# Kernel tuning notes

Measured on AMD Instinct MI355X. Metric: run time of the kernel, lower is better.

## Reference

```python
import jax, jax.numpy as jnp
import numpy as np

NUM_USERS = 100000
NUM_ITEMS = 100000
N = NUM_USERS + NUM_ITEMS
D = 64
E = 3200000


def setup_inputs() -> dict:
    key = jax.random.key(0)
    ks = jax.random.split(key, 8)
    edge_index = jax.random.randint(ks[0], (2, E), 0, N, dtype=jnp.int64)
    edge_weight = jax.random.uniform(ks[1], (E,), dtype=jnp.float32)
    user_emb = jax.random.normal(ks[2], (NUM_USERS, D), dtype=jnp.float32) * 0.1
    item_emb = jax.random.normal(ks[3], (NUM_ITEMS, D), dtype=jnp.float32) * 0.1
    s = 1.0 / np.sqrt(D)
    W1 = jax.random.uniform(ks[4], (D, D), dtype=jnp.float32, minval=-s, maxval=s)
    b1 = jax.random.uniform(ks[5], (D,), dtype=jnp.float32, minval=-s, maxval=s)
    W2 = jax.random.uniform(ks[6], (D, D), dtype=jnp.float32, minval=-s, maxval=s)
    b2 = jax.random.uniform(ks[7], (D,), dtype=jnp.float32, minval=-s, maxval=s)
    return {"edge_index": edge_index, "edge_weight": edge_weight,
            "user_emb": user_emb, "item_emb": item_emb,
            "W1": W1, "b1": b1, "W2": W2, "b2": b2}


def _gcn_layer(x, src, dst, edge_weight, W, b):
    # message: edge_weight * x[src]; aggregate: scatter-add at dst
    msg = edge_weight[:, None] * x[src]              # [E, D] gather + mul
    agg = jax.ops.segment_sum(msg, dst, num_segments=N)  # [N, D] scatter-add
    updated = (agg + x) * 0.5                        # residual average
    return updated @ W + b                           # linear


def reference(edge_index, edge_weight, user_emb, item_emb, W1, b1, W2, b2):
    src = edge_index[0]
    dst = edge_index[1]
    x = jnp.concatenate([user_emb, item_emb], axis=0)  # [N, D]
    x = _gcn_layer(x, src, dst, edge_weight, W1, b1)
    x = _gcn_layer(x, src, dst, edge_weight, W2, b2)
    return x
```

## Files before the change

kernel.cpp:

```cpp
#include <hip/hip_runtime.h>
#include <hip/hip_fp16.h>

#define NUM_USERS 100000
#define NN        200000
#define DD        64
#define EE        3200000
#define SCAN_CHUNK 2048
#define NB_SCAN   98

#define KB_   391
#define GSEG  512
#define EPS   (EE / GSEG)
#define MSEG  (KB_ * GSEG)

typedef _Float16 half8 __attribute__((ext_vector_type(8)));
typedef _Float16 half4 __attribute__((ext_vector_type(4)));
typedef float    f32x4 __attribute__((ext_vector_type(4)));

__global__ __launch_bounds__(256) void scan_partials_kernel(
    const int* __restrict__ counts, int* __restrict__ bsum, int len)
{
    __shared__ int s[256];
    const int t = threadIdx.x;
    int sum = 0;
    for (int i = t; i < SCAN_CHUNK; i += 256) {
        const int idx = blockIdx.x * SCAN_CHUNK + i;
        sum += (idx < len) ? counts[idx] : 0;
    }
    s[t] = sum; __syncthreads();
    for (int off = 128; off > 0; off >>= 1) {
        if (t < off) s[t] += s[t + off];
        __syncthreads();
    }
    if (t == 0) bsum[blockIdx.x] = s[0];
}

__global__ __launch_bounds__(128) void scan_top_kernel(int* __restrict__ bsum, int nb)
{
    __shared__ int s[128];
    const int t = threadIdx.x;
    const int v = (t < nb) ? bsum[t] : 0;
    s[t] = v; __syncthreads();
    for (int off = 1; off < 128; off <<= 1) {
        int add = (t >= off) ? s[t - off] : 0;
        __syncthreads();
        s[t] += add;
        __syncthreads();
    }
    if (t < nb) bsum[t] = s[t] - v;
}

__global__ __launch_bounds__(256) void scan_write_kernel(
    const int* __restrict__ counts, const int* __restrict__ bsum,
    int* __restrict__ out, int len)
{
    __shared__ int s[256];
    const int t    = threadIdx.x;
    const int base = blockIdx.x * SCAN_CHUNK + t * 8;
    int c[8], ex[8], run = 0;
#pragma unroll
    for (int j = 0; j < 8; ++j) {
        const int idx = base + j;
        c[j] = (idx < len) ? counts[idx] : 0;
        ex[j] = run; run += c[j];
    }
    s[t] = run; __syncthreads();
    for (int off = 1; off < 256; off <<= 1) {
        int add = (t >= off) ? s[t - off] : 0;
        __syncthreads();
        s[t] += add;
        __syncthreads();
    }
    const int thread_base = bsum[blockIdx.x] + s[t] - run;
#pragma unroll
    for (int j = 0; j < 8; ++j) {
        const int idx = base + j;
        if (idx < len) out[idx] = thread_base + ex[j];
    }
}

__global__ __launch_bounds__(256) void seg_hist_kernel(
    const int* __restrict__ ei, int* __restrict__ counts_seg)
{
    __shared__ int h[KB_];
    const int s = blockIdx.x;
    for (int k = threadIdx.x; k < KB_; k += 256) h[k] = 0;
    __syncthreads();
    const int base = s * EPS;
    for (int i = threadIdx.x; i < EPS; i += 256) {
        const int dst = __builtin_nontemporal_load(&ei[EE + base + i]);
        atomicAdd(&h[dst >> 9], 1);
    }
    __syncthreads();
    for (int k = threadIdx.x; k < KB_; k += 256)
        counts_seg[k * GSEG + s] = h[k];
}

__global__ __launch_bounds__(256) void append_kernel(
    const int* __restrict__ ei, const float* __restrict__ ew,
    const int* __restrict__ bofs, int2* __restrict__ etmp)
{
    __shared__ int fr[KB_];
    const int s = blockIdx.x;
    for (int k = threadIdx.x; k < KB_; k += 256) fr[k] = bofs[k * GSEG + s];
    __syncthreads();
    const int base = s * EPS;
    for (int i = threadIdx.x; i < EPS; i += 256) {
        const int e   = base + i;
        const int   src = __builtin_nontemporal_load(&ei[e]);
        const int   dst = __builtin_nontemporal_load(&ei[EE + e]);
        const float w   = __builtin_nontemporal_load(&ew[e]);
        const int k  = dst >> 9;
        const int dl = dst & 511;
        const int pos = atomicAdd(&fr[k], 1);
        etmp[pos] = make_int2(src | (dl << 18), __float_as_int(w));
    }
}

__global__ __launch_bounds__(256) void bucket_sort_kernel(
    const int2* __restrict__ etmp, const int* __restrict__ bofs,
    int2* __restrict__ edges, int* __restrict__ row_ptr)
{
    __shared__ int cnt[512];
    __shared__ int cur[512];
    __shared__ int part[256];
    const int k = blockIdx.x;
    const int t = threadIdx.x;
    cnt[t] = 0; cnt[t + 256] = 0;
    __syncthreads();
    const int beg = bofs[k * GSEG];
    const int end = (k == KB_ - 1) ? EE : bofs[(k + 1) * GSEG];
    for (int e = beg + t; e < end; e += 256)
        atomicAdd(&cnt[((unsigned)etmp[e].x) >> 18], 1);
    __syncthreads();
    const int c0 = cnt[2 * t], c1 = cnt[2 * t + 1];
    const int run = c0 + c1;
    part[t] = run; __syncthreads();
    for (int off = 1; off < 256; off <<= 1) {
        int add = (t >= off) ? part[t - off] : 0;
        __syncthreads();
        part[t] += add;
        __syncthreads();
    }
    const int base = beg + part[t] - run;
    cur[2 * t]     = base;
    cur[2 * t + 1] = base + c0;
    const int node0 = (k << 9) + 2 * t;
    if (node0 < NN)     row_ptr[node0]     = base;
    if (node0 + 1 < NN) row_ptr[node0 + 1] = base + c0;
    if (k == KB_ - 1 && t == 0) row_ptr[NN] = EE;
    __syncthreads();
    for (int e = beg + t; e < end; e += 256) {
        const int2 r  = etmp[e];
        const int  dl = ((unsigned)r.x) >> 18;
        const int  pos = atomicAdd(&cur[dl], 1);
        edges[pos] = make_int2((r.x & 0x3FFFF) << 7, r.y);
    }
}

__global__ __launch_bounds__(256) void convert_x_kernel(
    const float* __restrict__ xu, const float* __restrict__ xi,
    _Float16* __restrict__ xh)
{
    const int i = blockIdx.x * 256 + threadIdx.x;
    if (i >= NN * DD / 4) return;
    const float4 v = (i < NUM_USERS * DD / 4)
                       ? ((const float4*)xu)[i]
                       : ((const float4*)xi)[i - NUM_USERS * DD / 4];
    half4 o; o[0] = (_Float16)v.x; o[1] = (_Float16)v.y;
             o[2] = (_Float16)v.z; o[3] = (_Float16)v.w;
    ((half4*)xh)[i] = o;
}

__global__ __launch_bounds__(256) void convert_w_kernel(
    const float* __restrict__ W1, const float* __restrict__ W2,
    _Float16* __restrict__ Wt)
{
    const int idx = blockIdx.x * 256 + threadIdx.x;
    if (idx >= 2 * DD * DD) return;
    const int mat = idx >> 12, rem = idx & 4095, k = rem >> 6, n = rem & 63;
    const float* W = mat ? W2 : W1;
    Wt[mat * DD * DD + n * DD + k] = (_Float16)W[k * DD + n];
}

__global__ __launch_bounds__(256) void aggregate_kernel(
    const int2* __restrict__ edges, const int* __restrict__ row_ptr,
    const _Float16* __restrict__ xh, _Float16* __restrict__ u)
{
    const int wave = (blockIdx.x * 256 + threadIdx.x) >> 6;
    const int lane = threadIdx.x & 63;
    const unsigned lane2 = lane * 2;
    const int nbase = wave * 4;
    const char* xb = (const char*)xh;

    int bnd[5];
#pragma unroll
    for (int k = 0; k < 5; ++k)
        bnd[k] = __builtin_amdgcn_readfirstlane(row_ptr[nbase + k]);

    float acc[4];
#pragma unroll
    for (int k = 0; k < 4; ++k)
        acc[k] = (float)*(const _Float16*)(xb + ((unsigned)(nbase + k) << 7) + lane2);

    int e0 = bnd[0], e1 = bnd[1], e2 = bnd[2], e3 = bnd[3];
    const int f0 = bnd[1], f1 = bnd[2], f2 = bnd[3], f3 = bnd[4];

    while ((e0 + 4 <= f0) && (e1 + 4 <= f1) && (e2 + 4 <= f2) && (e3 + 4 <= f3)) {
        const int2 a0 = edges[e0 + 0], a1 = edges[e0 + 1];
        const int2 a2 = edges[e0 + 2], a3 = edges[e0 + 3];
        const int2 b0 = edges[e1 + 0], b1 = edges[e1 + 1];
        const int2 b2 = edges[e1 + 2], b3 = edges[e1 + 3];
        const int2 c0 = edges[e2 + 0], c1 = edges[e2 + 1];
        const int2 c2 = edges[e2 + 2], c3 = edges[e2 + 3];
        const int2 d0 = edges[e3 + 0], d1 = edges[e3 + 1];
        const int2 d2 = edges[e3 + 2], d3 = edges[e3 + 3];

        const float va0 = (float)*(const _Float16*)(xb + (unsigned)a0.x + lane2);
        const float va1 = (float)*(const _Float16*)(xb + (unsigned)a1.x + lane2);
        const float va2 = (float)*(const _Float16*)(xb + (unsigned)a2.x + lane2);
        const float va3 = (float)*(const _Float16*)(xb + (unsigned)a3.x + lane2);
        const float vb0 = (float)*(const _Float16*)(xb + (unsigned)b0.x + lane2);
        const float vb1 = (float)*(const _Float16*)(xb + (unsigned)b1.x + lane2);
        const float vb2 = (float)*(const _Float16*)(xb + (unsigned)b2.x + lane2);
        const float vb3 = (float)*(const _Float16*)(xb + (unsigned)b3.x + lane2);
        const float vc0 = (float)*(const _Float16*)(xb + (unsigned)c0.x + lane2);
        const float vc1 = (float)*(const _Float16*)(xb + (unsigned)c1.x + lane2);
        const float vc2 = (float)*(const _Float16*)(xb + (unsigned)c2.x + lane2);
        const float vc3 = (float)*(const _Float16*)(xb + (unsigned)c3.x + lane2);
        const float vd0 = (float)*(const _Float16*)(xb + (unsigned)d0.x + lane2);
        const float vd1 = (float)*(const _Float16*)(xb + (unsigned)d1.x + lane2);
        const float vd2 = (float)*(const _Float16*)(xb + (unsigned)d2.x + lane2);
        const float vd3 = (float)*(const _Float16*)(xb + (unsigned)d3.x + lane2);

        acc[0] = fmaf(__int_as_float(a0.y), va0, acc[0]);
        acc[0] = fmaf(__int_as_float(a1.y), va1, acc[0]);
        acc[0] = fmaf(__int_as_float(a2.y), va2, acc[0]);
        acc[0] = fmaf(__int_as_float(a3.y), va3, acc[0]);
        acc[1] = fmaf(__int_as_float(b0.y), vb0, acc[1]);
        acc[1] = fmaf(__int_as_float(b1.y), vb1, acc[1]);
        acc[1] = fmaf(__int_as_float(b2.y), vb2, acc[1]);
        acc[1] = fmaf(__int_as_float(b3.y), vb3, acc[1]);
        acc[2] = fmaf(__int_as_float(c0.y), vc0, acc[2]);
        acc[2] = fmaf(__int_as_float(c1.y), vc1, acc[2]);
        acc[2] = fmaf(__int_as_float(c2.y), vc2, acc[2]);
        acc[2] = fmaf(__int_as_float(c3.y), vc3, acc[2]);
        acc[3] = fmaf(__int_as_float(d0.y), vd0, acc[3]);
        acc[3] = fmaf(__int_as_float(d1.y), vd1, acc[3]);
        acc[3] = fmaf(__int_as_float(d2.y), vd2, acc[3]);
        acc[3] = fmaf(__int_as_float(d3.y), vd3, acc[3]);

        e0 += 4; e1 += 4; e2 += 4; e3 += 4;
    }

    {
        int e = e0;
        for (; e + 4 <= f0; e += 4) {
            const int2 r0 = edges[e + 0], r1 = edges[e + 1];
            const int2 r2 = edges[e + 2], r3 = edges[e + 3];
            const float v0 = (float)*(const _Float16*)(xb + (unsigned)r0.x + lane2);
            const float v1 = (float)*(const _Float16*)(xb + (unsigned)r1.x + lane2);
            const float v2 = (float)*(const _Float16*)(xb + (unsigned)r2.x + lane2);
            const float v3 = (float)*(const _Float16*)(xb + (unsigned)r3.x + lane2);
            acc[0] = fmaf(__int_as_float(r0.y), v0, acc[0]);
            acc[0] = fmaf(__int_as_float(r1.y), v1, acc[0]);
            acc[0] = fmaf(__int_as_float(r2.y), v2, acc[0]);
            acc[0] = fmaf(__int_as_float(r3.y), v3, acc[0]);
        }
        for (; e < f0; ++e) {
            const int2 p = edges[e];
            acc[0] = fmaf(__int_as_float(p.y),
                          (float)*(const _Float16*)(xb + (unsigned)p.x + lane2), acc[0]);
        }
    }
    {
        int e = e1;
        for (; e + 4 <= f1; e += 4) {
            const int2 r0 = edges[e + 0], r1 = edges[e + 1];
            const int2 r2 = edges[e + 2], r3 = edges[e + 3];
            const float v0 = (float)*(const _Float16*)(xb + (unsigned)r0.x + lane2);
            const float v1 = (float)*(const _Float16*)(xb + (unsigned)r1.x + lane2);
            const float v2 = (float)*(const _Float16*)(xb + (unsigned)r2.x + lane2);
            const float v3 = (float)*(const _Float16*)(xb + (unsigned)r3.x + lane2);
            acc[1] = fmaf(__int_as_float(r0.y), v0, acc[1]);
            acc[1] = fmaf(__int_as_float(r1.y), v1, acc[1]);
            acc[1] = fmaf(__int_as_float(r2.y), v2, acc[1]);
            acc[1] = fmaf(__int_as_float(r3.y), v3, acc[1]);
        }
        for (; e < f1; ++e) {
            const int2 p = edges[e];
            acc[1] = fmaf(__int_as_float(p.y),
                          (float)*(const _Float16*)(xb + (unsigned)p.x + lane2), acc[1]);
        }
    }
    {
        int e = e2;
        for (; e + 4 <= f2; e += 4) {
            const int2 r0 = edges[e + 0], r1 = edges[e + 1];
            const int2 r2 = edges[e + 2], r3 = edges[e + 3];
            const float v0 = (float)*(const _Float16*)(xb + (unsigned)r0.x + lane2);
            const float v1 = (float)*(const _Float16*)(xb + (unsigned)r1.x + lane2);
            const float v2 = (float)*(const _Float16*)(xb + (unsigned)r2.x + lane2);
            const float v3 = (float)*(const _Float16*)(xb + (unsigned)r3.x + lane2);
            acc[2] = fmaf(__int_as_float(r0.y), v0, acc[2]);
            acc[2] = fmaf(__int_as_float(r1.y), v1, acc[2]);
            acc[2] = fmaf(__int_as_float(r2.y), v2, acc[2]);
            acc[2] = fmaf(__int_as_float(r3.y), v3, acc[2]);
        }
        for (; e < f2; ++e) {
            const int2 p = edges[e];
            acc[2] = fmaf(__int_as_float(p.y),
                          (float)*(const _Float16*)(xb + (unsigned)p.x + lane2), acc[2]);
        }
    }
    {
        int e = e3;
        for (; e + 4 <= f3; e += 4) {
            const int2 r0 = edges[e + 0], r1 = edges[e + 1];
            const int2 r2 = edges[e + 2], r3 = edges[e + 3];
            const float v0 = (float)*(const _Float16*)(xb + (unsigned)r0.x + lane2);
            const float v1 = (float)*(const _Float16*)(xb + (unsigned)r1.x + lane2);
            const float v2 = (float)*(const _Float16*)(xb + (unsigned)r2.x + lane2);
            const float v3 = (float)*(const _Float16*)(xb + (unsigned)r3.x + lane2);
            acc[3] = fmaf(__int_as_float(r0.y), v0, acc[3]);
            acc[3] = fmaf(__int_as_float(r1.y), v1, acc[3]);
            acc[3] = fmaf(__int_as_float(r2.y), v2, acc[3]);
            acc[3] = fmaf(__int_as_float(r3.y), v3, acc[3]);
        }
        for (; e < f3; ++e) {
            const int2 p = edges[e];
            acc[3] = fmaf(__int_as_float(p.y),
                          (float)*(const _Float16*)(xb + (unsigned)p.x + lane2), acc[3]);
        }
    }

    char* ub = (char*)u;
#pragma unroll
    for (int k = 0; k < 4; ++k)
        *(_Float16*)(ub + ((unsigned)(nbase + k) << 7) + lane2) = (_Float16)(acc[k] * 0.5f);
}

template<bool HALF_OUT>
__global__ __launch_bounds__(256) void gemm64_kernel(
    const _Float16* __restrict__ u, const _Float16* __restrict__ Wt,
    const float* __restrict__ bias, void* __restrict__ outp)
{
    const int wid  = blockIdx.x * 4 + (threadIdx.x >> 6);
    const int lane = threadIdx.x & 63;
    const int m    = lane & 15;
    const int quad = lane >> 4;
    const size_t rowbase = (size_t)wid * 16;

    half8 bf[4][2];
#pragma unroll
    for (int c = 0; c < 4; ++c)
#pragma unroll
        for (int h = 0; h < 2; ++h)
            bf[c][h] = *(const half8*)(Wt + (size_t)(c * 16 + m) * DD + h * 32 + quad * 8);

    const half8 a0 = *(const half8*)(u + (rowbase + m) * DD +  0 + quad * 8);
    const half8 a1 = *(const half8*)(u + (rowbase + m) * DD + 32 + quad * 8);

    f32x4 acc[4];
#pragma unroll
    for (int c = 0; c < 4; ++c) {
        f32x4 z = {0.f, 0.f, 0.f, 0.f};
        z = __builtin_amdgcn_mfma_f32_16x16x32_f16(a0, bf[c][0], z, 0, 0, 0);
        z = __builtin_amdgcn_mfma_f32_16x16x32_f16(a1, bf[c][1], z, 0, 0, 0);
        acc[c] = z;
    }

#pragma unroll
    for (int c = 0; c < 4; ++c) {
        const float bv = bias[c * 16 + m];
#pragma unroll
        for (int r = 0; r < 4; ++r) {
            const size_t row = rowbase + quad * 4 + r;
            const float val = acc[c][r] + bv;
            if (HALF_OUT) ((_Float16*)outp)[row * DD + c * 16 + m] = (_Float16)val;
            else          ((float*)    outp)[row * DD + c * 16 + m] = val;
        }
    }
}

extern "C" void kernel_launch(void* const* d_in, const int* in_sizes, int n_in,
                              void* d_out, int out_size, void* d_ws, size_t ws_size,
                              hipStream_t stream) {
    const int*   edge_index  = (const int*)  d_in[0];
    const float* edge_weight = (const float*)d_in[1];
    const float* user_emb    = (const float*)d_in[2];
    const float* item_emb    = (const float*)d_in[3];
    const float* W1          = (const float*)d_in[4];
    const float* b1          = (const float*)d_in[5];
    const float* W2          = (const float*)d_in[6];
    const float* b2          = (const float*)d_in[7];
    float*       out         = (float*)d_out;

    char* ws = (char*)d_ws;
    _Float16* xh        = (_Float16*)(ws);
    _Float16* u         = (_Float16*)(ws + 25600000);
    int2*     etmp      = (int2*)    (ws + 25600000);
    int2*     edges     = (int2*)    (ws + 51200000);
    int*      row_ptr   = (int*)     (ws + 76800000);
    int*      cseg      = (int*)     (ws + 78400064);
    int*      bofs      = (int*)     (ws + 79200832);
    int*      bsum      = (int*)     (ws + 80001600);
    _Float16* Wt        = (_Float16*)(ws + 80002112);

    const int gemm_blocks = (NN / 16) / 4;
    const int agg_blocks  = NN / 16;

    seg_hist_kernel     <<<GSEG,    256, 0, stream>>>(edge_index, cseg);
    scan_partials_kernel<<<NB_SCAN, 256, 0, stream>>>(cseg, bsum, MSEG);
    scan_top_kernel     <<<1,       128, 0, stream>>>(bsum, NB_SCAN);
    scan_write_kernel   <<<NB_SCAN, 256, 0, stream>>>(cseg, bsum, bofs, MSEG);

    append_kernel      <<<GSEG, 256, 0, stream>>>(edge_index, edge_weight, bofs, etmp);
    bucket_sort_kernel <<<KB_,  256, 0, stream>>>(etmp, bofs, edges, row_ptr);

    convert_x_kernel<<<(NN * DD / 4 + 255) / 256, 256, 0, stream>>>(user_emb, item_emb, xh);
    convert_w_kernel<<<(2 * DD * DD + 255) / 256, 256, 0, stream>>>(W1, W2, Wt);

    aggregate_kernel<<<agg_blocks, 256, 0, stream>>>(edges, row_ptr, xh, u);
    gemm64_kernel<true><<<gemm_blocks, 256, 0, stream>>>(u, Wt, b1, (void*)xh);

    aggregate_kernel<<<agg_blocks, 256, 0, stream>>>(edges, row_ptr, xh, u);
    gemm64_kernel<false><<<gemm_blocks, 256, 0, stream>>>(u, Wt + DD * DD, b2, (void*)out);
}
```

Measured before the change: 446.9 us.

## Build CSR with global per-node atomics instead of two-level bucket sort

Replaces the segmented two-pass bucket sort (segment histogram, append into coarse buckets, per-bucket local sort) with a direct CSR build: a global atomic histogram over destination nodes, an exclusive scan into row_ptr and cursor arrays, and one scatter pass using a global atomicAdd per edge. This removes the intermediate etmp buffer pass and two kernels, trading them for 6.4M global atomics on random addresses. Edge order within a row becomes nondeterministic, and global atomic contention and latency may cost more than the LDS atomics they replace.

```diff
diff --git a/kernel.cpp b/kernel.cpp
--- a/kernel.cpp
+++ b/kernel.cpp
@@ -8,14 +8,20 @@
 #define SCAN_CHUNK 2048
 #define NB_SCAN   98
 
-#define KB_   391
-#define GSEG  512
-#define EPS   (EE / GSEG)
-#define MSEG  (KB_ * GSEG)
-
 typedef _Float16 half8 __attribute__((ext_vector_type(8)));
 typedef _Float16 half4 __attribute__((ext_vector_type(4)));
 typedef float    f32x4 __attribute__((ext_vector_type(4)));
+
+__global__ __launch_bounds__(256) void node_hist_kernel(
+    const int* __restrict__ ei, int* __restrict__ cnt)
+{
+    const int i = blockIdx.x * 256 + threadIdx.x;
+    const int4 d = ((const int4*)(ei + EE))[i];
+    atomicAdd(&cnt[d.x], 1);
+    atomicAdd(&cnt[d.y], 1);
+    atomicAdd(&cnt[d.z], 1);
+    atomicAdd(&cnt[d.w], 1);
+}
 
 __global__ __launch_bounds__(256) void scan_partials_kernel(
     const int* __restrict__ counts, int* __restrict__ bsum, int len)
@@ -52,7 +58,7 @@
 
 __global__ __launch_bounds__(256) void scan_write_kernel(
     const int* __restrict__ counts, const int* __restrict__ bsum,
-    int* __restrict__ out, int len)
+    int* __restrict__ row_ptr, int* __restrict__ cur, int len)
 {
     __shared__ int s[256];
     const int t    = threadIdx.x;
@@ -75,87 +81,26 @@
 #pragma unroll
     for (int j = 0; j < 8; ++j) {
         const int idx = base + j;
-        if (idx < len) out[idx] = thread_base + ex[j];
-    }
-}
-
-__global__ __launch_bounds__(256) void seg_hist_kernel(
-    const int* __restrict__ ei, int* __restrict__ counts_seg)
-{
-    __shared__ int h[KB_];
-    const int s = blockIdx.x;
-    for (int k = threadIdx.x; k < KB_; k += 256) h[k] = 0;
-    __syncthreads();
-    const int base = s * EPS;
-    for (int i = threadIdx.x; i < EPS; i += 256) {
-        const int dst = __builtin_nontemporal_load(&ei[EE + base + i]);
-        atomicAdd(&h[dst >> 9], 1);
-    }
-    __syncthreads();
-    for (int k = threadIdx.x; k < KB_; k += 256)
-        counts_seg[k * GSEG + s] = h[k];
-}
-
-__global__ __launch_bounds__(256) void append_kernel(
+        if (idx < len) {
+            const int v = thread_base + ex[j];
+            row_ptr[idx] = v;
+            cur[idx]     = v;
+        }
+    }
+    if (blockIdx.x == NB_SCAN - 1 && t == 255)
+        row_ptr[len] = bsum[blockIdx.x] + s[255];
+}
+
+__global__ __launch_bounds__(256) void scatter_kernel(
     const int* __restrict__ ei, const float* __restrict__ ew,
-    const int* __restrict__ bofs, int2* __restrict__ etmp)
-{
-    __shared__ int fr[KB_];
-    const int s = blockIdx.x;
-    for (int k = threadIdx.x; k < KB_; k += 256) fr[k] = bofs[k * GSEG + s];
-    __syncthreads();
-    const int base = s * EPS;
-    for (int i = threadIdx.x; i < EPS; i += 256) {
-        const int e   = base + i;
-        const int   src = __builtin_nontemporal_load(&ei[e]);
-        const int   dst = __builtin_nontemporal_load(&ei[EE + e]);
-        const float w   = __builtin_nontemporal_load(&ew[e]);
-        const int k  = dst >> 9;
-        const int dl = dst & 511;
-        const int pos = atomicAdd(&fr[k], 1);
-        etmp[pos] = make_int2(src | (dl << 18), __float_as_int(w));
-    }
-}
-
-__global__ __launch_bounds__(256) void bucket_sort_kernel(
-    const int2* __restrict__ etmp, const int* __restrict__ bofs,
-    int2* __restrict__ edges, int* __restrict__ row_ptr)
-{
-    __shared__ int cnt[512];
-    __shared__ int cur[512];
-    __shared__ int part[256];
-    const int k = blockIdx.x;
-    const int t = threadIdx.x;
-    cnt[t] = 0; cnt[t + 256] = 0;
-    __syncthreads();
-    const int beg = bofs[k * GSEG];
-    const int end = (k == KB_ - 1) ? EE : bofs[(k + 1) * GSEG];
-    for (int e = beg + t; e < end; e += 256)
-        atomicAdd(&cnt[((unsigned)etmp[e].x) >> 18], 1);
-    __syncthreads();
-    const int c0 = cnt[2 * t], c1 = cnt[2 * t + 1];
-    const int run = c0 + c1;
-    part[t] = run; __syncthreads();
-    for (int off = 1; off < 256; off <<= 1) {
-        int add = (t >= off) ? part[t - off] : 0;
-        __syncthreads();
-        part[t] += add;
-        __syncthreads();
-    }
-    const int base = beg + part[t] - run;
-    cur[2 * t]     = base;
-    cur[2 * t + 1] = base + c0;
-    const int node0 = (k << 9) + 2 * t;
-    if (node0 < NN)     row_ptr[node0]     = base;
-    if (node0 + 1 < NN) row_ptr[node0 + 1] = base + c0;
-    if (k == KB_ - 1 && t == 0) row_ptr[NN] = EE;
-    __syncthreads();
-    for (int e = beg + t; e < end; e += 256) {
-        const int2 r  = etmp[e];
-        const int  dl = ((unsigned)r.x) >> 18;
-        const int  pos = atomicAdd(&cur[dl], 1);
-        edges[pos] = make_int2((r.x & 0x3FFFF) << 7, r.y);
-    }
+    int* __restrict__ cur, int2* __restrict__ edges)
+{
+    const int i = blockIdx.x * 256 + threadIdx.x;
+    const int   src = ei[i];
+    const int   dst = ei[EE + i];
+    const float w   = ew[i];
+    const int pos = atomicAdd(&cur[dst], 1);
+    edges[pos] = make_int2(src << 7, __float_as_int(w));
 }
 
 __global__ __launch_bounds__(256) void convert_x_kernel(
@@ -399,24 +344,22 @@
     char* ws = (char*)d_ws;
     _Float16* xh        = (_Float16*)(ws);
     _Float16* u         = (_Float16*)(ws + 25600000);
-    int2*     etmp      = (int2*)    (ws + 25600000);
     int2*     edges     = (int2*)    (ws + 51200000);
     int*      row_ptr   = (int*)     (ws + 76800000);
-    int*      cseg      = (int*)     (ws + 78400064);
-    int*      bofs      = (int*)     (ws + 79200832);
+    int*      cur       = (int*)     (ws + 78400064);
+    int*      node_cnt  = (int*)     (ws + 79200832);
     int*      bsum      = (int*)     (ws + 80001600);
     _Float16* Wt        = (_Float16*)(ws + 80002112);
 
     const int gemm_blocks = (NN / 16) / 4;
     const int agg_blocks  = NN / 16;
 
-    seg_hist_kernel     <<<GSEG,    256, 0, stream>>>(edge_index, cseg);
-    scan_partials_kernel<<<NB_SCAN, 256, 0, stream>>>(cseg, bsum, MSEG);
-    scan_top_kernel     <<<1,       128, 0, stream>>>(bsum, NB_SCAN);
-    scan_write_kernel   <<<NB_SCAN, 256, 0, stream>>>(cseg, bsum, bofs, MSEG);
-
-    append_kernel      <<<GSEG, 256, 0, stream>>>(edge_index, edge_weight, bofs, etmp);
-    bucket_sort_kernel <<<KB_,  256, 0, stream>>>(etmp, bofs, edges, row_ptr);
+    hipMemsetAsync(node_cnt, 0, (size_t)NN * sizeof(int), stream);
+    node_hist_kernel    <<<EE / 1024, 256, 0, stream>>>(edge_index, node_cnt);
+    scan_partials_kernel<<<NB_SCAN,   256, 0, stream>>>(node_cnt, bsum, NN);
+    scan_top_kernel     <<<1,         128, 0, stream>>>(bsum, NB_SCAN);
+    scan_write_kernel   <<<NB_SCAN,   256, 0, stream>>>(node_cnt, bsum, row_ptr, cur, NN);
+    scatter_kernel      <<<EE / 256,  256, 0, stream>>>(edge_index, edge_weight, cur, edges);
 
     convert_x_kernel<<<(NN * DD / 4 + 255) / 256, 256, 0, stream>>>(user_emb, item_emb, xh);
     convert_w_kernel<<<(2 * DD * DD + 255) / 256, 256, 0, stream>>>(W1, W2, Wt);
```

Result: slower. 617.2 us (+38.1%).

## Fuse preprocessing kernels and restructure bucket offset scan to cut launches

Applied to the files above, without the earlier changes.

Merges the destination histogram with the x and W fp16 conversions into one prep kernel, and replaces the three-kernel global scan with a per-bucket scan over segments. Each consumer kernel (append and place) redundantly rescans the 391 bucket totals. The counts layout is transposed to segment-major, and the nontemporal loads on edge inputs become normal loads, so the second read of edge_index can hit cache. Kernel launch count drops from 10 to 6, at the cost of small redundant per-block scans.

```diff
diff --git a/kernel.cpp b/kernel.cpp
--- a/kernel.cpp
+++ b/kernel.cpp
@@ -5,111 +5,112 @@
 #define NN        200000
 #define DD        64
 #define EE        3200000
-#define SCAN_CHUNK 2048
-#define NB_SCAN   98
 
 #define KB_   391
 #define GSEG  512
 #define EPS   (EE / GSEG)
-#define MSEG  (KB_ * GSEG)
+#define CVX_BLOCKS 12500
+#define CVW_BLOCKS 32
 
 typedef _Float16 half8 __attribute__((ext_vector_type(8)));
 typedef _Float16 half4 __attribute__((ext_vector_type(4)));
 typedef float    f32x4 __attribute__((ext_vector_type(4)));
 
-__global__ __launch_bounds__(256) void scan_partials_kernel(
-    const int* __restrict__ counts, int* __restrict__ bsum, int len)
-{
-    __shared__ int s[256];
+__global__ __launch_bounds__(256) void prep_kernel(
+    const int* __restrict__ ei,
+    const float* __restrict__ xu, const float* __restrict__ xi,
+    const float* __restrict__ W1, const float* __restrict__ W2,
+    int* __restrict__ counts_seg, _Float16* __restrict__ xh,
+    _Float16* __restrict__ Wt)
+{
+    __shared__ int h[KB_];
+    const int b = blockIdx.x;
     const int t = threadIdx.x;
-    int sum = 0;
-    for (int i = t; i < SCAN_CHUNK; i += 256) {
-        const int idx = blockIdx.x * SCAN_CHUNK + i;
-        sum += (idx < len) ? counts[idx] : 0;
-    }
-    s[t] = sum; __syncthreads();
-    for (int off = 128; off > 0; off >>= 1) {
-        if (t < off) s[t] += s[t + off];
-        __syncthreads();
-    }
-    if (t == 0) bsum[blockIdx.x] = s[0];
-}
-
-__global__ __launch_bounds__(128) void scan_top_kernel(int* __restrict__ bsum, int nb)
-{
-    __shared__ int s[128];
+    if (b < GSEG) {
+        for (int k = t; k < KB_; k += 256) h[k] = 0;
+        __syncthreads();
+        const int base = b * EPS;
+        for (int i = t; i < EPS; i += 256) {
+            const int dst = ei[EE + base + i];
+            atomicAdd(&h[dst >> 9], 1);
+        }
+        __syncthreads();
+        for (int k = t; k < KB_; k += 256)
+            counts_seg[b * KB_ + k] = h[k];
+    } else if (b < GSEG + CVX_BLOCKS) {
+        const int i = (b - GSEG) * 256 + t;
+        const float4 v = (i < NUM_USERS * DD / 4)
+                           ? ((const float4*)xu)[i]
+                           : ((const float4*)xi)[i - NUM_USERS * DD / 4];
+        half4 o; o[0] = (_Float16)v.x; o[1] = (_Float16)v.y;
+                 o[2] = (_Float16)v.z; o[3] = (_Float16)v.w;
+        ((half4*)xh)[i] = o;
+    } else {
+        const int idx = (b - GSEG - CVX_BLOCKS) * 256 + t;
+        const int mat = idx >> 12, rem = idx & 4095, k = rem >> 6, n = rem & 63;
+        const float* W = mat ? W2 : W1;
+        Wt[mat * DD * DD + n * DD + k] = (_Float16)W[k * DD + n];
+    }
+}
+
+__global__ __launch_bounds__(256) void bscan_kernel(
+    int* __restrict__ counts_seg, int* __restrict__ btot)
+{
+    __shared__ int part[256];
+    const int k = blockIdx.x;
     const int t = threadIdx.x;
-    const int v = (t < nb) ? bsum[t] : 0;
-    s[t] = v; __syncthreads();
-    for (int off = 1; off < 128; off <<= 1) {
-        int add = (t >= off) ? s[t - off] : 0;
-        __syncthreads();
-        s[t] += add;
-        __syncthreads();
-    }
-    if (t < nb) bsum[t] = s[t] - v;
-}
-
-__global__ __launch_bounds__(256) void scan_write_kernel(
-    const int* __restrict__ counts, const int* __restrict__ bsum,
-    int* __restrict__ out, int len)
-{
-    __shared__ int s[256];
-    const int t    = threadIdx.x;
-    const int base = blockIdx.x * SCAN_CHUNK + t * 8;
-    int c[8], ex[8], run = 0;
-#pragma unroll
-    for (int j = 0; j < 8; ++j) {
-        const int idx = base + j;
-        c[j] = (idx < len) ? counts[idx] : 0;
-        ex[j] = run; run += c[j];
-    }
-    s[t] = run; __syncthreads();
+    const int c0 = counts_seg[(2 * t)     * KB_ + k];
+    const int c1 = counts_seg[(2 * t + 1) * KB_ + k];
+    const int run = c0 + c1;
+    part[t] = run; __syncthreads();
     for (int off = 1; off < 256; off <<= 1) {
-        int add = (t >= off) ? s[t - off] : 0;
-        __syncthreads();
-        s[t] += add;
-        __syncthreads();
-    }
-    const int thread_base = bsum[blockIdx.x] + s[t] - run;
-#pragma unroll
-    for (int j = 0; j < 8; ++j) {
-        const int idx = base + j;
-        if (idx < len) out[idx] = thread_base + ex[j];
-    }
-}
-
-__global__ __launch_bounds__(256) void seg_hist_kernel(
-    const int* __restrict__ ei, int* __restrict__ counts_seg)
-{
-    __shared__ int h[KB_];
-    const int s = blockIdx.x;
-    for (int k = threadIdx.x; k < KB_; k += 256) h[k] = 0;
-    __syncthreads();
-    const int base = s * EPS;
-    for (int i = threadIdx.x; i < EPS; i += 256) {
-        const int dst = __builtin_nontemporal_load(&ei[EE + base + i]);
-        atomicAdd(&h[dst >> 9], 1);
-    }
-    __syncthreads();
-    for (int k = threadIdx.x; k < KB_; k += 256)
-        counts_seg[k * GSEG + s] = h[k];
+        int add = (t >= off) ? part[t - off] : 0;
+        __syncthreads();
+        part[t] += add;
+        __syncthreads();
+    }
+    const int base = part[t] - run;
+    counts_seg[(2 * t)     * KB_ + k] = base;
+    counts_seg[(2 * t + 1) * KB_ + k] = base + c0;
+    if (t == 255) btot[k] = part[255];
 }
 
 __global__ __launch_bounds__(256) void append_kernel(
     const int* __restrict__ ei, const float* __restrict__ ew,
-    const int* __restrict__ bofs, int2* __restrict__ etmp)
-{
+    const int* __restrict__ counts_seg, const int* __restrict__ btot,
+    int2* __restrict__ etmp)
+{
+    __shared__ int sb[512];
+    __shared__ int part[256];
     __shared__ int fr[KB_];
     const int s = blockIdx.x;
-    for (int k = threadIdx.x; k < KB_; k += 256) fr[k] = bofs[k * GSEG + s];
+    const int t = threadIdx.x;
+    for (int j = t; j < 512; j += 256) sb[j] = (j < KB_) ? btot[j] : 0;
+    __syncthreads();
+    {
+        const int c0 = sb[2 * t], c1 = sb[2 * t + 1];
+        const int run = c0 + c1;
+        part[t] = run; __syncthreads();
+        for (int off = 1; off < 256; off <<= 1) {
+            int add = (t >= off) ? part[t - off] : 0;
+            __syncthreads();
+            part[t] += add;
+            __syncthreads();
+        }
+        const int base = part[t] - run;
+        sb[2 * t]     = base;
+        sb[2 * t + 1] = base + c0;
+    }
+    __syncthreads();
+    for (int k = t; k < KB_; k += 256)
+        fr[k] = sb[k] + counts_seg[s * KB_ + k];
     __syncthreads();
     const int base = s * EPS;
-    for (int i = threadIdx.x; i < EPS; i += 256) {
+    for (int i = t; i < EPS; i += 256) {
         const int e   = base + i;
-        const int   src = __builtin_nontemporal_load(&ei[e]);
-        const int   dst = __builtin_nontemporal_load(&ei[EE + e]);
-        const float w   = __builtin_nontemporal_load(&ew[e]);
+        const int   src = ei[e];
+        const int   dst = ei[EE + e];
+        const float w   = ew[e];
         const int k  = dst >> 9;
         const int dl = dst & 511;
         const int pos = atomicAdd(&fr[k], 1);
@@ -117,19 +118,37 @@
     }
 }
 
-__global__ __launch_bounds__(256) void bucket_sort_kernel(
-    const int2* __restrict__ etmp, const int* __restrict__ bofs,
+__global__ __launch_bounds__(256) void place_kernel(
+    const int2* __restrict__ etmp, const int* __restrict__ btot,
     int2* __restrict__ edges, int* __restrict__ row_ptr)
 {
+    __shared__ int sb[512];
+    __shared__ int part[256];
     __shared__ int cnt[512];
     __shared__ int cur[512];
-    __shared__ int part[256];
     const int k = blockIdx.x;
     const int t = threadIdx.x;
+    for (int j = t; j < 512; j += 256) sb[j] = (j < KB_) ? btot[j] : 0;
+    __syncthreads();
+    {
+        const int c0 = sb[2 * t], c1 = sb[2 * t + 1];
+        const int run = c0 + c1;
+        part[t] = run; __syncthreads();
+        for (int off = 1; off < 256; off <<= 1) {
+            int add = (t >= off) ? part[t - off] : 0;
+            __syncthreads();
+            part[t] += add;
+            __syncthreads();
+        }
+        const int base = part[t] - run;
+        sb[2 * t]     = base;
+        sb[2 * t + 1] = base + c0;
+    }
+    __syncthreads();
+    const int beg = sb[k];
+    const int end = (k == KB_ - 1) ? EE : sb[k + 1];
     cnt[t] = 0; cnt[t + 256] = 0;
     __syncthreads();
-    const int beg = bofs[k * GSEG];
-    const int end = (k == KB_ - 1) ? EE : bofs[(k + 1) * GSEG];
     for (int e = beg + t; e < end; e += 256)
         atomicAdd(&cnt[((unsigned)etmp[e].x) >> 18], 1);
     __syncthreads();
@@ -156,31 +175,6 @@
         const int  pos = atomicAdd(&cur[dl], 1);
         edges[pos] = make_int2((r.x & 0x3FFFF) << 7, r.y);
     }
-}
-
-__global__ __launch_bounds__(256) void convert_x_kernel(
-    const float* __restrict__ xu, const float* __restrict__ xi,
-    _Float16* __restrict__ xh)
-{
-    const int i = blockIdx.x * 256 + threadIdx.x;
-    if (i >= NN * DD / 4) return;
-    const float4 v = (i < NUM_USERS * DD / 4)
-                       ? ((const float4*)xu)[i]
-                       : ((const float4*)xi)[i - NUM_USERS * DD / 4];
-    half4 o; o[0] = (_Float16)v.x; o[1] = (_Float16)v.y;
-             o[2] = (_Float16)v.z; o[3] = (_Float16)v.w;
-    ((half4*)xh)[i] = o;
-}
-
-__global__ __launch_bounds__(256) void convert_w_kernel(
-    const float* __restrict__ W1, const float* __restrict__ W2,
-    _Float16* __restrict__ Wt)
-{
-    const int idx = blockIdx.x * 256 + threadIdx.x;
-    if (idx >= 2 * DD * DD) return;
-    const int mat = idx >> 12, rem = idx & 4095, k = rem >> 6, n = rem & 63;
-    const float* W = mat ? W2 : W1;
-    Wt[mat * DD * DD + n * DD + k] = (_Float16)W[k * DD + n];
 }
 
 __global__ __launch_bounds__(256) void aggregate_kernel(
@@ -402,24 +396,20 @@
     int2*     etmp      = (int2*)    (ws + 25600000);
     int2*     edges     = (int2*)    (ws + 51200000);
     int*      row_ptr   = (int*)     (ws + 76800000);
-    int*      cseg      = (int*)     (ws + 78400064);
-    int*      bofs      = (int*)     (ws + 79200832);
-    int*      bsum      = (int*)     (ws + 80001600);
-    _Float16* Wt        = (_Float16*)(ws + 80002112);
+    int*      counts_seg= (int*)     (ws + 77600064);
+    int*      btot      = (int*)     (ws + 78400832);
+    _Float16* Wt        = (_Float16*)(ws + 78402432);
 
     const int gemm_blocks = (NN / 16) / 4;
     const int agg_blocks  = NN / 16;
-
-    seg_hist_kernel     <<<GSEG,    256, 0, stream>>>(edge_index, cseg);
-    scan_partials_kernel<<<NB_SCAN, 256, 0, stream>>>(cseg, bsum, MSEG);
-    scan_top_kernel     <<<1,       128, 0, stream>>>(bsum, NB_SCAN);
-    scan_write_kernel   <<<NB_SCAN, 256, 0, stream>>>(cseg, bsum, bofs, MSEG);
-
-    append_kernel      <<<GSEG, 256, 0, stream>>>(edge_index, edge_weight, bofs, etmp);
-    bucket_sort_kernel <<<KB_,  256, 0, stream>>>(etmp, bofs, edges, row_ptr);
-
-    convert_x_kernel<<<(NN * DD / 4 + 255) / 256, 256, 0, stream>>>(user_emb, item_emb, xh);
-    convert_w_kernel<<<(2 * DD * DD + 255) / 256, 256, 0, stream>>>(W1, W2, Wt);
+    const int prep_blocks = GSEG + CVX_BLOCKS + CVW_BLOCKS;
+
+    prep_kernel  <<<prep_blocks, 256, 0, stream>>>(edge_index, user_emb, item_emb,
+                                                   W1, W2, counts_seg, xh, Wt);
+    bscan_kernel <<<KB_,  256, 0, stream>>>(counts_seg, btot);
+    append_kernel<<<GSEG, 256, 0, stream>>>(edge_index, edge_weight,
+                                            counts_seg, btot, etmp);
+    place_kernel <<<KB_,  256, 0, stream>>>(etmp, btot, edges, row_ptr);
 
     aggregate_kernel<<<agg_blocks, 256, 0, stream>>>(edges, row_ptr, xh, u);
     gemm64_kernel<true><<<gemm_blocks, 256, 0, stream>>>(u, Wt, b1, (void*)xh);
```

After: 430.9 us. -3.6%, faster.
